# Kernel tuning notes

Hardware: AMD Instinct MI355X
Metric: run time of the kernel (lower is better)

## Reference

```python
import jax, jax.numpy as jnp
import numpy as np

DIM = 1024
HEADS = 16
HEAD_DIM = DIM // HEADS
SCALE = HEAD_DIM ** -0.5


def setup_inputs() -> dict:
    key = jax.random.key(0)
    ks = jax.random.split(key, 8)
    B, N, C = 2, 2048, DIM
    std = 0.02
    return {
        "x": jax.random.normal(ks[0], (B, N, C), dtype=jnp.float32),
        "e": jax.random.normal(ks[1], (B, N, C), dtype=jnp.float32),
        "W_qkv": jax.random.normal(ks[2], (C, 3 * C), dtype=jnp.float32) * std,
        "W_s": jax.random.normal(ks[3], (C, C), dtype=jnp.float32) * std,
        "W_gate": jax.random.normal(ks[4], (C, C), dtype=jnp.float32) * std,
        "W_proj": jax.random.normal(ks[5], (C, C), dtype=jnp.float32) * std,
        "b_proj": jax.random.normal(ks[6], (C,), dtype=jnp.float32) * std,
    }


def reference(x, e, W_qkv, W_s, W_gate, W_proj, b_proj):
    B, N, C = x.shape
    H, D = HEADS, HEAD_DIM
    # qkv: [B,N,3C] -> [3,B,H,N,D]
    qkv = (x @ W_qkv).reshape(B, N, 3, H, D).transpose(2, 0, 3, 1, 4)
    q, k, v = qkv[0], qkv[1], qkv[2]
    gate = x @ W_gate  # [B,N,C]
    # s bias fused into keys: [B,H,N,D]
    s = (e @ W_s).reshape(B, N, H, D).transpose(0, 2, 1, 3)
    attn = jnp.einsum("bhnd,bhmd->bhnm", q, k + s) * SCALE
    attn = jax.nn.softmax(attn, axis=-1)
    out = jnp.einsum("bhnm,bhmd->bhnd", attn, v)  # [B,H,N,D]
    out = out.transpose(0, 2, 1, 3).reshape(B, N, C)
    out = out * gate
    return out @ W_proj + b_proj
```

## Files before the change

kernel.cpp:

```cpp
#include <hip/hip_runtime.h>
#include <hip/hip_bf16.h>

#define SCALE 0.125f
#define QSCALE 0.18033688f
#define RESCALE_THR 8.0f

typedef __attribute__((ext_vector_type(8))) __bf16 bf16x8;
typedef __attribute__((ext_vector_type(4))) float f32x4;
typedef __attribute__((ext_vector_type(4))) short s16x4;
typedef __hip_bfloat16 bf16;

__device__ __forceinline__ void gl_lds16(const bf16* g, bf16* l) {
  __builtin_amdgcn_global_load_lds(
      (const __attribute__((address_space(1))) void*)g,
      (__attribute__((address_space(3))) void*)l, 16, 0, 0);
}

__device__ __forceinline__ float fexp2(float x) {
#if __has_builtin(__builtin_amdgcn_exp2f)
  return __builtin_amdgcn_exp2f(x);
#else
  return exp2f(x);
#endif
}

__device__ __forceinline__ unsigned cvt_pk_bf16(float lo, float hi) {
  unsigned r;
  asm("v_cvt_pk_bf16_f32 %0, %1, %2" : "=v"(r) : "v"(lo), "v"(hi));
  return r;
}

__device__ __forceinline__ f32x4 zf4() {
  f32x4 v; v[0] = 0.f; v[1] = 0.f; v[2] = 0.f; v[3] = 0.f; return v;
}

__global__ __launch_bounds__(256) void conv_bf16_k(const float* __restrict__ in,
                                                   bf16* __restrict__ out, int n4) {
  int i = blockIdx.x * 256 + threadIdx.x;
  if (i >= n4) return;
  const float4 v = reinterpret_cast<const float4*>(in)[i];
  union { bf16 h4[4]; s16x4 s; } u;
  u.h4[0] = __float2bfloat16(v.x);
  u.h4[1] = __float2bfloat16(v.y);
  u.h4[2] = __float2bfloat16(v.z);
  u.h4[3] = __float2bfloat16(v.w);
  reinterpret_cast<s16x4*>(out)[i] = u.s;
}

__global__ __launch_bounds__(256) void transp_k(const float* __restrict__ W,
                                                bf16* __restrict__ Wt, int K, int N) {
  __shared__ float t[32][33];
  const int tx = threadIdx.x, ty = threadIdx.y;
  const int n0 = blockIdx.x * 32, k0 = blockIdx.y * 32;
#pragma unroll
  for (int i = 0; i < 4; ++i)
    t[ty + 8 * i][tx] = W[(k0 + ty + 8 * i) * N + n0 + tx];
  __syncthreads();
#pragma unroll
  for (int i = 0; i < 4; ++i)
    Wt[(n0 + ty + 8 * i) * K + k0 + tx] = __float2bfloat16(t[tx][ty + 8 * i]);
}

struct GemmP {
  const bf16* A;
  const bf16* B0;
  const bf16* B1;
  const bf16* sT;
  bf16 *q, *k, *vt, *gate, *obf;
  float* out;
  const float* bias;
};

__global__ __launch_bounds__(512, 2) void gemm256_k(GemmP p) {
  constexpr int K = 1024;
  constexpr int NT = 16;
  __shared__ bf16 AB[2][2][256 * 64];
  const int tid = threadIdx.x;
  const int wid = tid >> 6, lane = tid & 63;
  const int l15 = lane & 15, l4 = lane >> 4;
  const int wr = wid >> 2, wc = wid & 3;

  const int bid0 = blockIdx.y * 16 + blockIdx.x;
  const int bid = (bid0 & 7) * 32 + (bid0 >> 3);
  const int m0 = (bid >> 4) * 256, n0 = (bid & 15) * 256;

  const bf16* Arow = p.A + (size_t)m0 * K;
  const bf16* Brow = (n0 >= 3072) ? p.B1 + (size_t)(n0 - 3072) * K
                                  : p.B0 + (size_t)n0 * K;

  f32x4 acc[8][4];
#pragma unroll
  for (int m = 0; m < 8; ++m)
#pragma unroll
    for (int n = 0; n < 4; ++n) acc[m][n] = zf4();

  const int srow = tid >> 3, sc = tid & 7;
  auto stageA = [&](int b, int kt) {
#pragma unroll
    for (int s = 0; s < 4; ++s) {
      const int r = s * 64 + srow;
      const int c2 = sc ^ (r & 7);
      gl_lds16(Arow + (size_t)r * K + kt * 64 + c2 * 8, &AB[b][0][r * 64 + sc * 8]);
    }
  };
  auto stageB = [&](int b, int kt) {
#pragma unroll
    for (int s = 0; s < 4; ++s) {
      const int r = s * 64 + srow;
      const int c2 = sc ^ (r & 7);
      gl_lds16(Brow + (size_t)r * K + kt * 64 + c2 * 8, &AB[b][1][r * 64 + sc * 8]);
    }
  };

  stageA(0, 0);
  stageB(0, 0);
  __syncthreads();
  int cur = 0;

  for (int kt = 0; kt < NT; ++kt) {
    bf16x8 bfv[4][2];
#pragma unroll
    for (int q = 0; q < 4; ++q) {
      bf16x8 af[2][2];
#pragma unroll
      for (int mm = 0; mm < 2; ++mm) {
        const int row = wr * 128 + (q * 2 + mm) * 16 + l15;
#pragma unroll
        for (int ks = 0; ks < 2; ++ks)
          af[mm][ks] = *reinterpret_cast<const bf16x8*>(
              &AB[cur][0][row * 64 + ((ks * 4 + l4) ^ (row & 7)) * 8]);
      }
      if (q == 0) {
#pragma unroll
        for (int n = 0; n < 4; ++n) {
          const int row = wc * 64 + n * 16 + l15;
#pragma unroll
          for (int ks = 0; ks < 2; ++ks)
            bfv[n][ks] = *reinterpret_cast<const bf16x8*>(
                &AB[cur][1][row * 64 + ((ks * 4 + l4) ^ (row & 7)) * 8]);
        }
      }
      if (q == 0 && kt + 1 < NT) stageA(cur ^ 1, kt + 1);
      if (q == 1 && kt + 1 < NT) stageB(cur ^ 1, kt + 1);

      __builtin_amdgcn_s_barrier();
      __builtin_amdgcn_s_setprio(1);
#pragma unroll
      for (int mm = 0; mm < 2; ++mm)
#pragma unroll
        for (int n = 0; n < 4; ++n)
#pragma unroll
          for (int ks = 0; ks < 2; ++ks)
            acc[q * 2 + mm][n] = __builtin_amdgcn_mfma_f32_16x16x32_bf16(
                af[mm][ks], bfv[n][ks], acc[q * 2 + mm][n], 0, 0, 0);
      __builtin_amdgcn_s_setprio(0);
      __builtin_amdgcn_s_barrier();
    }
    asm volatile("s_waitcnt vmcnt(0)" ::: "memory");
    __builtin_amdgcn_s_barrier();
    cur ^= 1;
  }

#pragma unroll
  for (int m = 0; m < 8; ++m) {
    const int gr0 = m0 + wr * 128 + m * 16 + l4 * 4;
    const int bb = gr0 >> 11;
    const int nn0 = gr0 & 2047;
#pragma unroll
    for (int n = 0; n < 4; ++n) {
      const int gc = n0 + wc * 64 + n * 16 + l15;
      if (gc < 3072) {
        const int t = gc >> 10, hd = gc & 1023;
        const int h = hd >> 6, d = hd & 63;
        const int base = ((bb * 16 + h) * 2048 + nn0) * 64 + d;
        if (t == 0) {
#pragma unroll
          for (int r = 0; r < 4; ++r)
            p.q[base + r * 64] = __float2bfloat16(acc[m][n][r] * QSCALE);
        } else if (t == 1) {
#pragma unroll
          for (int r = 0; r < 4; ++r)
            p.k[base + r * 64] =
                __float2bfloat16(acc[m][n][r] + __bfloat162float(p.sT[base + r * 64]));
        } else {
          union { bf16 h4[4]; s16x4 s; } u;
#pragma unroll
          for (int r = 0; r < 4; ++r) u.h4[r] = __float2bfloat16(acc[m][n][r]);
          *reinterpret_cast<s16x4*>(&p.vt[((bb * 16 + h) * 64 + d) * 2048 + nn0]) = u.s;
        }
      } else {
        const int gcc = gc - 3072;
#pragma unroll
        for (int r = 0; r < 4; ++r)
          p.gate[(gr0 + r) * 1024 + gcc] = __float2bfloat16(acc[m][n][r]);
      }
    }
  }
}

template <int EPI>
__global__ __launch_bounds__(256) void gemm2_k(GemmP p) {
  constexpr int K = 1024;
  __shared__ bf16 As[64 * 32];
  __shared__ bf16 Bs[128 * 32];
  const int tid = threadIdx.x;
  const int wid = tid >> 6, lane = tid & 63;
  const int l15 = lane & 15, l4 = lane >> 4;
  const int wc = wid;
  const int m0 = blockIdx.y * 64, n0 = blockIdx.x * 128;
  const bf16* Arow = p.A + m0 * K;
  const bf16* Brow = p.B0 + n0 * K;

  f32x4 acc[4][2];
#pragma unroll
  for (int m = 0; m < 4; ++m)
#pragma unroll
    for (int n = 0; n < 2; ++n) acc[m][n] = zf4();

  const int srowA = tid >> 2, skc = tid & 3;
  for (int kt = 0; kt < K; kt += 32) {
    gl_lds16(Arow + srowA * K + kt + skc * 8, As + wid * 512);
#pragma unroll
    for (int it = 0; it < 2; ++it)
      gl_lds16(Brow + (it * 64 + srowA) * K + kt + skc * 8, Bs + it * 2048 + wid * 512);
    __syncthreads();
    bf16x8 af[4], bfr[2];
#pragma unroll
    for (int m = 0; m < 4; ++m)
      af[m] = *reinterpret_cast<const bf16x8*>(&As[(m * 16 + l15) * 32 + 8 * l4]);
#pragma unroll
    for (int n = 0; n < 2; ++n)
      bfr[n] = *reinterpret_cast<const bf16x8*>(&Bs[(wc * 32 + n * 16 + l15) * 32 + 8 * l4]);
#pragma unroll
    for (int m = 0; m < 4; ++m)
#pragma unroll
      for (int n = 0; n < 2; ++n)
        acc[m][n] = __builtin_amdgcn_mfma_f32_16x16x32_bf16(af[m], bfr[n], acc[m][n], 0, 0, 0);
    __syncthreads();
  }

#pragma unroll
  for (int m = 0; m < 4; ++m) {
    const int gr0 = m0 + m * 16 + l4 * 4;
    const int bb = gr0 >> 11;
    const int nn0 = gr0 & 2047;
#pragma unroll
    for (int n = 0; n < 2; ++n) {
      const int gc = n0 + wc * 32 + n * 16 + l15;
      if (EPI == 0) {
        const int h = gc >> 6, d = gc & 63;
        bf16* dst = p.obf + ((bb * 16 + h) * 2048 + nn0) * 64 + d;
#pragma unroll
        for (int r = 0; r < 4; ++r) dst[r * 64] = __float2bfloat16(acc[m][n][r]);
      } else {
        const float bias = p.bias[gc];
#pragma unroll
        for (int r = 0; r < 4; ++r) p.out[(gr0 + r) * 1024 + gc] = acc[m][n][r] + bias;
      }
    }
  }
}

__global__ __launch_bounds__(256) void flash_k(const bf16* __restrict__ qT,
                                               const bf16* __restrict__ kTb,
                                               const bf16* __restrict__ vTt,
                                               const bf16* __restrict__ gateb,
                                               bf16* __restrict__ attng) {
  __shared__ bf16 Ks[2][64 * 64];
  __shared__ bf16 Vs[2][64 * 64];
  const int tid = threadIdx.x;
  const int wid = tid >> 6, lane = tid & 63;
  const int l15 = lane & 15, l4 = lane >> 4;
  const int hbit = lane >> 5;
  const int qt = blockIdx.x, bh = blockIdx.y;
  const int qr0 = qt * 64 + wid * 16;
  const bf16* qbase = qT + (bh * 2048 + qr0) * 64;
  const bf16x8 qf0 = *reinterpret_cast<const bf16x8*>(&qbase[l15 * 64 + 8 * l4]);
  const bf16x8 qf1 = *reinterpret_cast<const bf16x8*>(&qbase[l15 * 64 + 32 + 8 * l4]);
  const bf16* kbase = kTb + bh * 2048 * 64;
  const bf16* vbase = vTt + bh * 64 * 2048;
  const int srcQ0 = (((lane & 16) << 1) | (lane & 15)) << 2;
  const int srcQ1 = srcQ0 | 64;

  f32x4 o[4];
#pragma unroll
  for (int i = 0; i < 4; ++i) o[i] = zf4();
  float mrun = -1e30f, lrun = 0.f;
  const int srow = tid >> 3, sc = tid & 7;

  auto stage = [&](int b, int kt) {
#pragma unroll
    for (int it = 0; it < 2; ++it) {
      const int row = it * 32 + srow;
      const int c2 = sc ^ (row & 7);
      gl_lds16(kbase + (kt * 64 + row) * 64 + c2 * 8, &Ks[b][it * 2048 + wid * 512]);
      gl_lds16(vbase + row * 2048 + kt * 64 + c2 * 8, &Vs[b][it * 2048 + wid * 512]);
    }
  };

  stage(0, 0);
  __syncthreads();
  int cur = 0;

  for (int kt = 0; kt < 32; ++kt) {
    if (kt < 31) stage(cur ^ 1, kt + 1);

    f32x4 sa[4];
#pragma unroll
    for (int n = 0; n < 4; ++n) sa[n] = zf4();
    __builtin_amdgcn_s_setprio(1);
#pragma unroll
    for (int kk = 0; kk < 2; ++kk) {
      const bf16x8 qv = kk ? qf1 : qf0;
#pragma unroll
      for (int n = 0; n < 4; ++n) {
        const int key = n * 16 + l15;
        const bf16x8 kv = *reinterpret_cast<const bf16x8*>(
            &Ks[cur][key * 64 + ((kk * 4 + l4) ^ (key & 7)) * 8]);
        sa[n] = __builtin_amdgcn_mfma_f32_16x16x32_bf16(kv, qv, sa[n], 0, 0, 0);
      }
    }
    __builtin_amdgcn_s_setprio(0);

    float mt = sa[0][0];
#pragma unroll
    for (int n = 0; n < 4; ++n)
#pragma unroll
      for (int r = 0; r < 4; ++r) mt = fmaxf(mt, sa[n][r]);
    mt = fmaxf(mt, __shfl_xor(mt, 16, 64));
    mt = fmaxf(mt, __shfl_xor(mt, 32, 64));

    const bool upd = !__all(mt <= mrun + RESCALE_THR);
    float fac = 1.f;
    if (upd) {
      const float mn = fmaxf(mrun, mt);
      fac = fexp2(mrun - mn);
      mrun = mn;
    }

    float p[4][4];
    float psum = 0.f;
#pragma unroll
    for (int n = 0; n < 4; ++n)
#pragma unroll
      for (int r = 0; r < 4; ++r) {
        p[n][r] = fexp2(sa[n][r] - mrun);
        psum += p[n][r];
      }
    psum += __shfl_xor(psum, 16, 64);
    psum += __shfl_xor(psum, 32, 64);
    if (upd) {
      lrun = lrun * fac + psum;
#pragma unroll
      for (int nd = 0; nd < 4; ++nd)
#pragma unroll
        for (int r = 0; r < 4; ++r) o[nd][r] *= fac;
    } else {
      lrun += psum;
    }

    int Cp[4][2];
#pragma unroll
    for (int n = 0; n < 4; ++n) {
      Cp[n][0] = (int)cvt_pk_bf16(p[n][0], p[n][1]);
      Cp[n][1] = (int)cvt_pk_bf16(p[n][2], p[n][3]);
    }

    __builtin_amdgcn_s_setprio(1);
#pragma unroll
    for (int kk = 0; kk < 2; ++kk) {
      const int x0 = __builtin_amdgcn_ds_bpermute(srcQ0, Cp[2 * kk][0]);
      const int x1 = __builtin_amdgcn_ds_bpermute(srcQ0, Cp[2 * kk + 1][0]);
      const int y0 = __builtin_amdgcn_ds_bpermute(srcQ0, Cp[2 * kk][1]);
      const int y1 = __builtin_amdgcn_ds_bpermute(srcQ0, Cp[2 * kk + 1][1]);
      const int z0 = __builtin_amdgcn_ds_bpermute(srcQ1, Cp[2 * kk][0]);
      const int z1 = __builtin_amdgcn_ds_bpermute(srcQ1, Cp[2 * kk + 1][0]);
      const int t0 = __builtin_amdgcn_ds_bpermute(srcQ1, Cp[2 * kk][1]);
      const int t1 = __builtin_amdgcn_ds_bpermute(srcQ1, Cp[2 * kk + 1][1]);
      union { int u[4]; bf16x8 v; } pw;
      pw.u[0] = hbit ? x1 : x0;
      pw.u[1] = hbit ? y1 : y0;
      pw.u[2] = hbit ? z1 : z0;
      pw.u[3] = hbit ? t1 : t0;
#pragma unroll
      for (int nd = 0; nd < 4; ++nd) {
        const int d = nd * 16 + l15;
        const bf16x8 vv = *reinterpret_cast<const bf16x8*>(
            &Vs[cur][d * 64 + ((kk * 4 + l4) ^ (d & 7)) * 8]);
        o[nd] = __builtin_amdgcn_mfma_f32_16x16x32_bf16(vv, pw.v, o[nd], 0, 0, 0);
      }
    }
    __builtin_amdgcn_s_setprio(0);

    __syncthreads();
    cur ^= 1;
  }

  const int bb = bh >> 4, h = bh & 15;
  const int grow = bb * 2048 + qr0 + l15;
  const float inv = 1.0f / lrun;
#pragma unroll
  for (int nd = 0; nd < 4; ++nd) {
    const int gi = grow * 1024 + h * 64 + nd * 16 + l4 * 4;
    union { s16x4 s; bf16 h4[4]; } gu, ou;
    gu.s = *reinterpret_cast<const s16x4*>(&gateb[gi]);
#pragma unroll
    for (int r = 0; r < 4; ++r)
      ou.h4[r] = __float2bfloat16(o[nd][r] * inv * __bfloat162float(gu.h4[r]));
    *reinterpret_cast<s16x4*>(&attng[gi]) = ou.s;
  }
}

extern "C" void kernel_launch(void* const* d_in, const int* in_sizes, int n_in,
                              void* d_out, int out_size, void* d_ws, size_t ws_size,
                              hipStream_t stream) {
  const float* x = (const float*)d_in[0];
  const float* e = (const float*)d_in[1];
  const float* Wqkv = (const float*)d_in[2];
  const float* Ws = (const float*)d_in[3];
  const float* Wgate = (const float*)d_in[4];
  const float* Wproj = (const float*)d_in[5];
  const float* bproj = (const float*)d_in[6];
  float* out = (float*)d_out;

  char* w = (char*)d_ws;
  auto carve = [&](size_t bytes) -> void* {
    void* p = (void*)w;
    w += (bytes + 255) & ~size_t(255);
    return p;
  };
  bf16* xbf    = (bf16*)carve(4096UL * 1024 * 2);
  bf16* ebf    = (bf16*)carve(4096UL * 1024 * 2);
  bf16* Wqkvt  = (bf16*)carve(3072UL * 1024 * 2);
  bf16* Wst    = (bf16*)carve(1024UL * 1024 * 2);
  bf16* Wgatet = (bf16*)carve(1024UL * 1024 * 2);
  bf16* Wprojt = (bf16*)carve(1024UL * 1024 * 2);
  bf16* kTb    = (bf16*)carve(32UL * 2048 * 64 * 2);
  bf16* vTt    = (bf16*)carve(32UL * 64 * 2048 * 2);
  bf16* sT     = (bf16*)carve(32UL * 2048 * 64 * 2);
  bf16* gateb  = (bf16*)carve(4096UL * 1024 * 2);
  bf16* qT     = ebf;
  bf16* attng  = sT;

  conv_bf16_k<<<4096, 256, 0, stream>>>(x, xbf, 1048576);
  conv_bf16_k<<<4096, 256, 0, stream>>>(e, ebf, 1048576);
  transp_k<<<dim3(96, 32), dim3(32, 8), 0, stream>>>(Wqkv, Wqkvt, 1024, 3072);
  transp_k<<<dim3(32, 32), dim3(32, 8), 0, stream>>>(Ws, Wst, 1024, 1024);
  transp_k<<<dim3(32, 32), dim3(32, 8), 0, stream>>>(Wgate, Wgatet, 1024, 1024);
  transp_k<<<dim3(32, 32), dim3(32, 8), 0, stream>>>(Wproj, Wprojt, 1024, 1024);

  GemmP ps{};
  ps.A = ebf; ps.B0 = Wst; ps.obf = sT;
  gemm2_k<0><<<dim3(8, 64), 256, 0, stream>>>(ps);

  GemmP pq{};
  pq.A = xbf; pq.B0 = Wqkvt; pq.B1 = Wgatet; pq.sT = sT;
  pq.q = qT; pq.k = kTb; pq.vt = vTt; pq.gate = gateb;
  gemm256_k<<<dim3(16, 16), 512, 0, stream>>>(pq);

  flash_k<<<dim3(32, 32), 256, 0, stream>>>(qT, kTb, vTt, gateb, attng);

  GemmP pp{};
  pp.A = attng; pp.B0 = Wprojt; pp.out = out; pp.bias = bproj;
  gemm2_k<2><<<dim3(8, 64), 256, 0, stream>>>(pp);
}
```

Before: 279.7 us.

## Process two query groups per wave in flash attention and batch prep kernels

Each flash-attention wave now handles 32 query rows as two 16-row groups, so every K and V fragment read from LDS feeds two MFMAs. The block covers 128 queries and the grid is halved. This cuts LDS traffic and K/V staging per query, at the cost of more registers and half as many workgroups. The separate bf16 conversion kernels and the four weight-transpose kernels are each merged into one launch to reduce launch overhead.

```diff
diff --git a/kernel.cpp b/kernel.cpp
--- a/kernel.cpp
+++ b/kernel.cpp
@@ -34,10 +34,14 @@
   f32x4 v; v[0] = 0.f; v[1] = 0.f; v[2] = 0.f; v[3] = 0.f; return v;
 }
 
-__global__ __launch_bounds__(256) void conv_bf16_k(const float* __restrict__ in,
-                                                   bf16* __restrict__ out, int n4) {
-  int i = blockIdx.x * 256 + threadIdx.x;
-  if (i >= n4) return;
+__global__ __launch_bounds__(256) void conv2_bf16_k(const float* __restrict__ a,
+                                                    const float* __restrict__ b,
+                                                    bf16* __restrict__ oa,
+                                                    bf16* __restrict__ ob) {
+  const int bi = blockIdx.x;
+  const float* in = (bi < 4096) ? a : b;
+  bf16* out = (bi < 4096) ? oa : ob;
+  const int i = ((bi < 4096) ? bi : bi - 4096) * 256 + threadIdx.x;
   const float4 v = reinterpret_cast<const float4*>(in)[i];
   union { bf16 h4[4]; s16x4 s; } u;
   u.h4[0] = __float2bfloat16(v.x);
@@ -47,18 +51,24 @@
   reinterpret_cast<s16x4*>(out)[i] = u.s;
 }
 
-__global__ __launch_bounds__(256) void transp_k(const float* __restrict__ W,
-                                                bf16* __restrict__ Wt, int K, int N) {
+struct TranspP { const float* s[4]; bf16* d[4]; };
+__global__ __launch_bounds__(256) void transp_all_k(TranspP tp) {
   __shared__ float t[32][33];
+  const int z = blockIdx.z;
+  const int j = (z < 3) ? 0 : z - 2;
+  const int coff = (z < 3) ? (z << 10) : 0;
+  const int Nsrc = (j == 0) ? 3072 : 1024;
+  const float* W = tp.s[j];
+  bf16* dst = tp.d[j] + (size_t)((z < 3) ? z : 0) * 1024 * 1024;
   const int tx = threadIdx.x, ty = threadIdx.y;
   const int n0 = blockIdx.x * 32, k0 = blockIdx.y * 32;
 #pragma unroll
   for (int i = 0; i < 4; ++i)
-    t[ty + 8 * i][tx] = W[(k0 + ty + 8 * i) * N + n0 + tx];
+    t[ty + 8 * i][tx] = W[(k0 + ty + 8 * i) * Nsrc + coff + n0 + tx];
   __syncthreads();
 #pragma unroll
   for (int i = 0; i < 4; ++i)
-    Wt[(n0 + ty + 8 * i) * K + k0 + tx] = __float2bfloat16(t[tx][ty + 8 * i]);
+    dst[(n0 + ty + 8 * i) * 1024 + k0 + tx] = __float2bfloat16(t[tx][ty + 8 * i]);
 }
 
 struct GemmP {
@@ -273,19 +283,26 @@
   const int l15 = lane & 15, l4 = lane >> 4;
   const int hbit = lane >> 5;
   const int qt = blockIdx.x, bh = blockIdx.y;
-  const int qr0 = qt * 64 + wid * 16;
+  const int qr0 = qt * 128 + wid * 32;
   const bf16* qbase = qT + (bh * 2048 + qr0) * 64;
-  const bf16x8 qf0 = *reinterpret_cast<const bf16x8*>(&qbase[l15 * 64 + 8 * l4]);
-  const bf16x8 qf1 = *reinterpret_cast<const bf16x8*>(&qbase[l15 * 64 + 32 + 8 * l4]);
+  bf16x8 qf[2][2];
+#pragma unroll
+  for (int g = 0; g < 2; ++g)
+#pragma unroll
+    for (int kk = 0; kk < 2; ++kk)
+      qf[g][kk] = *reinterpret_cast<const bf16x8*>(
+          &qbase[(g * 16 + l15) * 64 + kk * 32 + 8 * l4]);
   const bf16* kbase = kTb + bh * 2048 * 64;
   const bf16* vbase = vTt + bh * 64 * 2048;
   const int srcQ0 = (((lane & 16) << 1) | (lane & 15)) << 2;
   const int srcQ1 = srcQ0 | 64;
 
-  f32x4 o[4];
-#pragma unroll
-  for (int i = 0; i < 4; ++i) o[i] = zf4();
-  float mrun = -1e30f, lrun = 0.f;
+  f32x4 o[2][4];
+#pragma unroll
+  for (int g = 0; g < 2; ++g)
+#pragma unroll
+    for (int i = 0; i < 4; ++i) o[g][i] = zf4();
+  float mrun[2] = {-1e30f, -1e30f}, lrun[2] = {0.f, 0.f};
   const int srow = tid >> 3, sc = tid & 7;
 
   auto stage = [&](int b, int kt) {
@@ -305,89 +322,109 @@
   for (int kt = 0; kt < 32; ++kt) {
     if (kt < 31) stage(cur ^ 1, kt + 1);
 
-    f32x4 sa[4];
-#pragma unroll
-    for (int n = 0; n < 4; ++n) sa[n] = zf4();
+    f32x4 sa[2][4];
+#pragma unroll
+    for (int g = 0; g < 2; ++g)
+#pragma unroll
+      for (int n = 0; n < 4; ++n) sa[g][n] = zf4();
     __builtin_amdgcn_s_setprio(1);
 #pragma unroll
     for (int kk = 0; kk < 2; ++kk) {
-      const bf16x8 qv = kk ? qf1 : qf0;
 #pragma unroll
       for (int n = 0; n < 4; ++n) {
         const int key = n * 16 + l15;
         const bf16x8 kv = *reinterpret_cast<const bf16x8*>(
             &Ks[cur][key * 64 + ((kk * 4 + l4) ^ (key & 7)) * 8]);
-        sa[n] = __builtin_amdgcn_mfma_f32_16x16x32_bf16(kv, qv, sa[n], 0, 0, 0);
+#pragma unroll
+        for (int g = 0; g < 2; ++g)
+          sa[g][n] = __builtin_amdgcn_mfma_f32_16x16x32_bf16(kv, qf[g][kk], sa[g][n], 0, 0, 0);
       }
     }
     __builtin_amdgcn_s_setprio(0);
 
-    float mt = sa[0][0];
-#pragma unroll
-    for (int n = 0; n < 4; ++n)
-#pragma unroll
-      for (int r = 0; r < 4; ++r) mt = fmaxf(mt, sa[n][r]);
-    mt = fmaxf(mt, __shfl_xor(mt, 16, 64));
-    mt = fmaxf(mt, __shfl_xor(mt, 32, 64));
-
-    const bool upd = !__all(mt <= mrun + RESCALE_THR);
-    float fac = 1.f;
+    float mt[2];
+#pragma unroll
+    for (int g = 0; g < 2; ++g) {
+      float m = sa[g][0][0];
+#pragma unroll
+      for (int n = 0; n < 4; ++n)
+#pragma unroll
+        for (int r = 0; r < 4; ++r) m = fmaxf(m, sa[g][n][r]);
+      m = fmaxf(m, __shfl_xor(m, 16, 64));
+      mt[g] = fmaxf(m, __shfl_xor(m, 32, 64));
+    }
+
+    const int okg = (mt[0] <= mrun[0] + RESCALE_THR) & (mt[1] <= mrun[1] + RESCALE_THR);
+    const bool upd = !__all(okg);
+    float fac[2] = {1.f, 1.f};
     if (upd) {
-      const float mn = fmaxf(mrun, mt);
-      fac = fexp2(mrun - mn);
-      mrun = mn;
-    }
-
-    float p[4][4];
-    float psum = 0.f;
-#pragma unroll
-    for (int n = 0; n < 4; ++n)
-#pragma unroll
-      for (int r = 0; r < 4; ++r) {
-        p[n][r] = fexp2(sa[n][r] - mrun);
-        psum += p[n][r];
-      }
-    psum += __shfl_xor(psum, 16, 64);
-    psum += __shfl_xor(psum, 32, 64);
-    if (upd) {
-      lrun = lrun * fac + psum;
-#pragma unroll
-      for (int nd = 0; nd < 4; ++nd)
-#pragma unroll
-        for (int r = 0; r < 4; ++r) o[nd][r] *= fac;
-    } else {
-      lrun += psum;
-    }
-
-    int Cp[4][2];
-#pragma unroll
-    for (int n = 0; n < 4; ++n) {
-      Cp[n][0] = (int)cvt_pk_bf16(p[n][0], p[n][1]);
-      Cp[n][1] = (int)cvt_pk_bf16(p[n][2], p[n][3]);
+#pragma unroll
+      for (int g = 0; g < 2; ++g) {
+        const float mn = fmaxf(mrun[g], mt[g]);
+        fac[g] = fexp2(mrun[g] - mn);
+        mrun[g] = mn;
+      }
+    }
+
+    int Cp[2][4][2];
+#pragma unroll
+    for (int g = 0; g < 2; ++g) {
+      float psum = 0.f;
+      float p[4][4];
+#pragma unroll
+      for (int n = 0; n < 4; ++n)
+#pragma unroll
+        for (int r = 0; r < 4; ++r) {
+          p[n][r] = fexp2(sa[g][n][r] - mrun[g]);
+          psum += p[n][r];
+        }
+      psum += __shfl_xor(psum, 16, 64);
+      psum += __shfl_xor(psum, 32, 64);
+      if (upd) {
+        lrun[g] = lrun[g] * fac[g] + psum;
+#pragma unroll
+        for (int nd = 0; nd < 4; ++nd)
+#pragma unroll
+          for (int r = 0; r < 4; ++r) o[g][nd][r] *= fac[g];
+      } else {
+        lrun[g] += psum;
+      }
+#pragma unroll
+      for (int n = 0; n < 4; ++n) {
+        Cp[g][n][0] = (int)cvt_pk_bf16(p[n][0], p[n][1]);
+        Cp[g][n][1] = (int)cvt_pk_bf16(p[n][2], p[n][3]);
+      }
     }
 
     __builtin_amdgcn_s_setprio(1);
 #pragma unroll
     for (int kk = 0; kk < 2; ++kk) {
-      const int x0 = __builtin_amdgcn_ds_bpermute(srcQ0, Cp[2 * kk][0]);
-      const int x1 = __builtin_amdgcn_ds_bpermute(srcQ0, Cp[2 * kk + 1][0]);
-      const int y0 = __builtin_amdgcn_ds_bpermute(srcQ0, Cp[2 * kk][1]);
-      const int y1 = __builtin_amdgcn_ds_bpermute(srcQ0, Cp[2 * kk + 1][1]);
-      const int z0 = __builtin_amdgcn_ds_bpermute(srcQ1, Cp[2 * kk][0]);
-      const int z1 = __builtin_amdgcn_ds_bpermute(srcQ1, Cp[2 * kk + 1][0]);
-      const int t0 = __builtin_amdgcn_ds_bpermute(srcQ1, Cp[2 * kk][1]);
-      const int t1 = __builtin_amdgcn_ds_bpermute(srcQ1, Cp[2 * kk + 1][1]);
-      union { int u[4]; bf16x8 v; } pw;
-      pw.u[0] = hbit ? x1 : x0;
-      pw.u[1] = hbit ? y1 : y0;
-      pw.u[2] = hbit ? z1 : z0;
-      pw.u[3] = hbit ? t1 : t0;
+      bf16x8 pw[2];
+#pragma unroll
+      for (int g = 0; g < 2; ++g) {
+        const int x0 = __builtin_amdgcn_ds_bpermute(srcQ0, Cp[g][2 * kk][0]);
+        const int x1 = __builtin_amdgcn_ds_bpermute(srcQ0, Cp[g][2 * kk + 1][0]);
+        const int y0 = __builtin_amdgcn_ds_bpermute(srcQ0, Cp[g][2 * kk][1]);
+        const int y1 = __builtin_amdgcn_ds_bpermute(srcQ0, Cp[g][2 * kk + 1][1]);
+        const int z0 = __builtin_amdgcn_ds_bpermute(srcQ1, Cp[g][2 * kk][0]);
+        const int z1 = __builtin_amdgcn_ds_bpermute(srcQ1, Cp[g][2 * kk + 1][0]);
+        const int t0 = __builtin_amdgcn_ds_bpermute(srcQ1, Cp[g][2 * kk][1]);
+        const int t1 = __builtin_amdgcn_ds_bpermute(srcQ1, Cp[g][2 * kk + 1][1]);
+        union { int u[4]; bf16x8 v; } u;
+        u.u[0] = hbit ? x1 : x0;
+        u.u[1] = hbit ? y1 : y0;
+        u.u[2] = hbit ? z1 : z0;
+        u.u[3] = hbit ? t1 : t0;
+        pw[g] = u.v;
+      }
 #pragma unroll
       for (int nd = 0; nd < 4; ++nd) {
         const int d = nd * 16 + l15;
         const bf16x8 vv = *reinterpret_cast<const bf16x8*>(
             &Vs[cur][d * 64 + ((kk * 4 + l4) ^ (d & 7)) * 8]);
-        o[nd] = __builtin_amdgcn_mfma_f32_16x16x32_bf16(vv, pw.v, o[nd], 0, 0, 0);
+#pragma unroll
+        for (int g = 0; g < 2; ++g)
+          o[g][nd] = __builtin_amdgcn_mfma_f32_16x16x32_bf16(vv, pw[g], o[g][nd], 0, 0, 0);
       }
     }
     __builtin_amdgcn_s_setprio(0);
@@ -397,17 +434,20 @@
   }
 
   const int bb = bh >> 4, h = bh & 15;
-  const int grow = bb * 2048 + qr0 + l15;
-  const float inv = 1.0f / lrun;
-#pragma unroll
-  for (int nd = 0; nd < 4; ++nd) {
-    const int gi = grow * 1024 + h * 64 + nd * 16 + l4 * 4;
-    union { s16x4 s; bf16 h4[4]; } gu, ou;
-    gu.s = *reinterpret_cast<const s16x4*>(&gateb[gi]);
-#pragma unroll
-    for (int r = 0; r < 4; ++r)
-      ou.h4[r] = __float2bfloat16(o[nd][r] * inv * __bfloat162float(gu.h4[r]));
-    *reinterpret_cast<s16x4*>(&attng[gi]) = ou.s;
+#pragma unroll
+  for (int g = 0; g < 2; ++g) {
+    const int grow = bb * 2048 + qr0 + g * 16 + l15;
+    const float inv = 1.0f / lrun[g];
+#pragma unroll
+    for (int nd = 0; nd < 4; ++nd) {
+      const int gi = grow * 1024 + h * 64 + nd * 16 + l4 * 4;
+      union { s16x4 s; bf16 h4[4]; } gu, ou;
+      gu.s = *reinterpret_cast<const s16x4*>(&gateb[gi]);
+#pragma unroll
+      for (int r = 0; r < 4; ++r)
+        ou.h4[r] = __float2bfloat16(o[g][nd][r] * inv * __bfloat162float(gu.h4[r]));
+      *reinterpret_cast<s16x4*>(&attng[gi]) = ou.s;
+    }
   }
 }
 
@@ -442,12 +482,12 @@
   bf16* qT     = ebf;
   bf16* attng  = sT;
 
-  conv_bf16_k<<<4096, 256, 0, stream>>>(x, xbf, 1048576);
-  conv_bf16_k<<<4096, 256, 0, stream>>>(e, ebf, 1048576);
-  transp_k<<<dim3(96, 32), dim3(32, 8), 0, stream>>>(Wqkv, Wqkvt, 1024, 3072);
-  transp_k<<<dim3(32, 32), dim3(32, 8), 0, stream>>>(Ws, Wst, 1024, 1024);
-  transp_k<<<dim3(32, 32), dim3(32, 8), 0, stream>>>(Wgate, Wgatet, 1024, 1024);
-  transp_k<<<dim3(32, 32), dim3(32, 8), 0, stream>>>(Wproj, Wprojt, 1024, 1024);
+  conv2_bf16_k<<<8192, 256, 0, stream>>>(x, e, xbf, ebf);
+
+  TranspP tp{};
+  tp.s[0] = Wqkv; tp.s[1] = Ws; tp.s[2] = Wgate; tp.s[3] = Wproj;
+  tp.d[0] = Wqkvt; tp.d[1] = Wst; tp.d[2] = Wgatet; tp.d[3] = Wprojt;
+  transp_all_k<<<dim3(32, 32, 6), dim3(32, 8), 0, stream>>>(tp);
 
   GemmP ps{};
   ps.A = ebf; ps.B0 = Wst; ps.obf = sT;
@@ -458,7 +498,7 @@
   pq.q = qT; pq.k = kTb; pq.vt = vTt; pq.gate = gateb;
   gemm256_k<<<dim3(16, 16), 512, 0, stream>>>(pq);
 
-  flash_k<<<dim3(32, 32), 256, 0, stream>>>(qT, kTb, vTt, gateb, attng);
+  flash_k<<<dim3(16, 32), 256, 0, stream>>>(qT, kTb, vTt, gateb, attng);
 
   GemmP pp{};
   pp.A = attng; pp.B0 = Wprojt; pp.out = out; pp.bias = bproj;
```

After: 268.7 us. 1.04x faster.
